# Optimization experiments

Hardware: AMD Instinct MI355X
Metric: run time of the kernel (lower is better)

## Reference

```python
import jax, jax.numpy as jnp
import numpy as np


def setup_inputs() -> dict:
    key = jax.random.key(0)
    k_x, k_w = jax.random.split(key)
    x = jax.random.normal(k_x, (4096, 4096), dtype=jnp.float32)
    weight = jax.random.uniform(k_w, (7, 7), dtype=jnp.float32)
    bias = jnp.zeros((1,), dtype=jnp.float32)
    return {"x": x, "weight": weight, "bias": bias}


def reference(x, weight, bias):
    # Valid 2D cross-correlation (no kernel flip), matching corr2d, plus scalar bias.
    # lax.conv_general_dilated performs cross-correlation by default.
    lhs = x[None, None, :, :]            # [1, 1, H, W]
    rhs = weight[None, None, :, :]       # [1, 1, kh, kw]
    y = jax.lax.conv_general_dilated(
        lhs, rhs,
        window_strides=(1, 1),
        padding="VALID",
        dimension_numbers=("NCHW", "OIHW", "NCHW"),
    )[0, 0]                              # [H-kh+1, W-kw+1]
    return y + bias[0]
```

## Files before the change

### kernel.cpp

```cpp
#include <hip/hip_runtime.h>

#define WI 4096
#define HI 4096
#define WO 4090
#define HO 4090
#define TH 12
#define IH 18
#define IWP 520
#define CPR 130
#define ACH (12*CPR)
#define NCH (IH*CPR)

__device__ __forceinline__ void gl_lds16(const float* g, float* l) {
    __builtin_amdgcn_global_load_lds(
        (const __attribute__((address_space(1))) void*)g,
        (__attribute__((address_space(3))) void*)l, 16, 0, 0);
}

__global__ __launch_bounds__(256, 4) void conv7x7(
    const float* __restrict__ x, const float* __restrict__ wgt,
    const float* __restrict__ bias, float* __restrict__ out)
{
    __shared__ float lds[IH * IWP];

    const int tid = threadIdx.x;
    const int x0  = blockIdx.x * 512;
    const int y0  = blockIdx.y * TH;

    float Wt[49];
    #pragma unroll
    for (int i = 0; i < 49; ++i) Wt[i] = wgt[i];
    const float bb = bias[0];

    const int cx  = 2 * tid;
    const int gx  = x0 + cx;
    const bool stok = (gx + 1 < WO);

    auto stage = [&](int c0, int n) {
        for (int c = c0 + tid; c < c0 + n; c += 256) {
            const int rr = c / CPR;
            const int c4 = c - rr * CPR;
            int gy = y0 + rr;       gy  = gy  < HI ? gy : HI - 1;
            int gxs = x0 + c4 * 4;  gxs = gxs <= WI - 4 ? gxs : WI - 4;
            gl_lds16(x + (size_t)gy * WI + gxs, lds + c * 4);
        }
    };

    float a0[7], a1[7];
    #pragma unroll
    for (int s = 0; s < 7; ++s) { a0[s] = 0.f; a1[s] = 0.f; }

    #define DOROW(r)                                                        \
    {                                                                       \
        const float* lrow_ = lds + (r) * IWP + cx;                          \
        const float2 q0 = *(const float2*)(lrow_ + 0);                      \
        const float2 q1 = *(const float2*)(lrow_ + 2);                      \
        const float2 q2 = *(const float2*)(lrow_ + 4);                      \
        const float2 q3 = *(const float2*)(lrow_ + 6);                      \
        const float f_[8] = {q0.x,q0.y,q1.x,q1.y,q2.x,q2.y,q3.x,q3.y};      \
        _Pragma("unroll")                                                   \
        for (int ky = 0; ky < 7; ++ky) {                                    \
            const int oy = (r) - ky;                            \
            if (oy >= 0 && oy < TH) {                                       \
                const int s = oy % 7;                           \
                _Pragma("unroll")                                           \
                for (int kx = 0; kx < 7; ++kx) {                            \
                    const float w_ = Wt[ky * 7 + kx];                       \
                    a0[s] += w_ * f_[kx];                                   \
                    a1[s] += w_ * f_[kx + 1];                               \
                }                                                           \
            }                                                               \
        }                                                                   \
        if ((r) >= 6) {                                         \
            const int oy = (r) - 6;                                         \
            const int s  = oy % 7;                              \
            const int gy = y0 + oy;                                         \
            if (stok && gy < HO) {                                          \
                float2 o_; o_.x = a0[s] + bb; o_.y = a1[s] + bb;            \
                *(float2*)(out + (size_t)gy * WO + gx) = o_;                \
            }                                                               \
            a0[s] = 0.f; a1[s] = 0.f;                                       \
        }                                                                   \
    }

    stage(0, ACH);
    __syncthreads();

    stage(ACH, NCH - ACH);

    #pragma unroll
    for (int r = 0; r < 12; ++r) DOROW(r)

    __syncthreads();

    #pragma unroll
    for (int r = 12; r < 18; ++r) DOROW(r)

    #undef DOROW
}

extern "C" void kernel_launch(void* const* d_in, const int* in_sizes, int n_in,
                              void* d_out, int out_size, void* d_ws, size_t ws_size,
                              hipStream_t stream) {
    const float* x = (const float*)d_in[0];
    const float* w = (const float*)d_in[1];
    const float* b = (const float*)d_in[2];
    float* out = (float*)d_out;
    dim3 grid(8, 341);
    conv7x7<<<grid, 256, 0, stream>>>(x, w, b, out);
}
```

Measured before the change: 36.68 us.

## Widen per-thread output to 4 columns and shrink tile height to 6 rows

Each thread now computes 4 adjacent output columns instead of 2, and each block covers 1024 columns by 6 output rows instead of 512 by 12. Loading a wider row segment per thread reuses each LDS read across more outputs, so fewer LDS reads are needed per output. The cost is that each block now stages 12 input rows to produce only 6 output rows, so the vertical halo overhead in staged input rises from 1.5x to 2x. The larger accumulator set raises register use, and occupancy hints drop from 4 to 3 blocks per CU.

```diff
diff --git a/kernel.cpp b/kernel.cpp
--- a/kernel.cpp
+++ b/kernel.cpp
@@ -4,11 +4,11 @@
 #define HI 4096
 #define WO 4090
 #define HO 4090
-#define TH 12
-#define IH 18
-#define IWP 520
-#define CPR 130
-#define ACH (12*CPR)
+#define TH 6
+#define IH 12
+#define IWP 1032
+#define CPR 258
+#define ACH (8*CPR)
 #define NCH (IH*CPR)
 
 __device__ __forceinline__ void gl_lds16(const float* g, float* l) {
@@ -17,14 +17,14 @@
         (__attribute__((address_space(3))) void*)l, 16, 0, 0);
 }
 
-__global__ __launch_bounds__(256, 4) void conv7x7(
+__global__ __launch_bounds__(256, 3) void conv7x7(
     const float* __restrict__ x, const float* __restrict__ wgt,
     const float* __restrict__ bias, float* __restrict__ out)
 {
     __shared__ float lds[IH * IWP];
 
     const int tid = threadIdx.x;
-    const int x0  = blockIdx.x * 512;
+    const int x0  = blockIdx.x * 1024;
     const int y0  = blockIdx.y * TH;
 
     float Wt[49];
@@ -32,9 +32,10 @@
     for (int i = 0; i < 49; ++i) Wt[i] = wgt[i];
     const float bb = bias[0];
 
-    const int cx  = 2 * tid;
+    const int cx  = 4 * tid;
     const int gx  = x0 + cx;
-    const bool stok = (gx + 1 < WO);
+    const bool st0 = (gx + 1 < WO);
+    const bool st1 = (gx + 3 < WO);
 
     auto stage = [&](int c0, int n) {
         for (int c = c0 + tid; c < c0 + n; c += 256) {
@@ -46,40 +47,44 @@
         }
     };
 
-    float a0[7], a1[7];
+    float acc[TH][4];
     #pragma unroll
-    for (int s = 0; s < 7; ++s) { a0[s] = 0.f; a1[s] = 0.f; }
+    for (int o = 0; o < TH; ++o)
+        #pragma unroll
+        for (int c = 0; c < 4; ++c) acc[o][c] = 0.f;
 
     #define DOROW(r)                                                        \
     {                                                                       \
         const float* lrow_ = lds + (r) * IWP + cx;                          \
-        const float2 q0 = *(const float2*)(lrow_ + 0);                      \
-        const float2 q1 = *(const float2*)(lrow_ + 2);                      \
-        const float2 q2 = *(const float2*)(lrow_ + 4);                      \
-        const float2 q3 = *(const float2*)(lrow_ + 6);                      \
-        const float f_[8] = {q0.x,q0.y,q1.x,q1.y,q2.x,q2.y,q3.x,q3.y};      \
+        const float4 q0 = *(const float4*)(lrow_ + 0);                      \
+        const float4 q1 = *(const float4*)(lrow_ + 4);                      \
+        const float2 q2 = *(const float2*)(lrow_ + 8);                      \
+        const float f_[10] = {q0.x,q0.y,q0.z,q0.w,                          \
+                              q1.x,q1.y,q1.z,q1.w,q2.x,q2.y};               \
         _Pragma("unroll")                                                   \
         for (int ky = 0; ky < 7; ++ky) {                                    \
             const int oy = (r) - ky;                            \
             if (oy >= 0 && oy < TH) {                                       \
-                const int s = oy % 7;                           \
                 _Pragma("unroll")                                           \
                 for (int kx = 0; kx < 7; ++kx) {                            \
                     const float w_ = Wt[ky * 7 + kx];                       \
-                    a0[s] += w_ * f_[kx];                                   \
-                    a1[s] += w_ * f_[kx + 1];                               \
+                    acc[oy][0] += w_ * f_[kx + 0];                          \
+                    acc[oy][1] += w_ * f_[kx + 1];                          \
+                    acc[oy][2] += w_ * f_[kx + 2];                          \
+                    acc[oy][3] += w_ * f_[kx + 3];                          \
                 }                                                           \
             }                                                               \
         }                                                                   \
         if ((r) >= 6) {                                         \
-            const int oy = (r) - 6;                                         \
-            const int s  = oy % 7;                              \
+            const int oy = (r) - 6;                \
             const int gy = y0 + oy;                                         \
-            if (stok && gy < HO) {                                          \
-                float2 o_; o_.x = a0[s] + bb; o_.y = a1[s] + bb;            \
-                *(float2*)(out + (size_t)gy * WO + gx) = o_;                \
+            if (gy < HO) {                                                  \
+                float* po_ = out + (size_t)gy * WO + gx;                    \
+                if (st0) *(float2*)(po_ + 0) =                              \
+                    make_float2(acc[oy][0] + bb, acc[oy][1] + bb);          \
+                if (st1) *(float2*)(po_ + 2) =                              \
+                    make_float2(acc[oy][2] + bb, acc[oy][3] + bb);          \
             }                                                               \
-            a0[s] = 0.f; a1[s] = 0.f;                                       \
         }                                                                   \
     }
 
@@ -89,12 +94,12 @@
     stage(ACH, NCH - ACH);
 
     #pragma unroll
-    for (int r = 0; r < 12; ++r) DOROW(r)
+    for (int r = 0; r < 8; ++r) DOROW(r)
 
     __syncthreads();
 
     #pragma unroll
-    for (int r = 12; r < 18; ++r) DOROW(r)
+    for (int r = 8; r < 12; ++r) DOROW(r)
 
     #undef DOROW
 }
@@ -106,6 +111,6 @@
     const float* w = (const float*)d_in[1];
     const float* b = (const float*)d_in[2];
     float* out = (float*)d_out;
-    dim3 grid(8, 341);
+    dim3 grid(4, 682);
     conv7x7<<<grid, 256, 0, stream>>>(x, w, b, out);
 }
```

After: 45.54 us. +24.2%, slower.
